# Kernel tuning notes

Measured on AMD Instinct MI355X. Metric: run time of the kernel, lower is better.

## Reference

```python
import jax, jax.numpy as jnp
import numpy as np

ATTRACTION_W = 1.0
REPULSION_W = 1.0
BETA_POS_W = 1.0
BETA_NEG_W = 0.5
K_INST = 256  # max number of distinct instance ids (slice ids)


def setup_inputs() -> dict:
    key = jax.random.key(0)
    B, N, D, K = 4, 65536, 256, K_INST
    k1, k2, k3 = jax.random.split(key, 3)
    beta = jax.random.normal(k1, (B, N, 1), jnp.float32)
    embed = jax.random.normal(k2, (B, N, D), jnp.float32)
    sid = jax.random.randint(k3, (B, N), -1, K)  # -1 = background
    # force exactly one condensation point per instance: hit i (<K) -> sid=i, is_cp
    sid = sid.at[:, :K].set(jnp.broadcast_to(jnp.arange(K), (B, K)))
    is_cp = jnp.zeros((B, N), bool).at[:, :K].set(True)
    return {"beta": beta, "embed": embed, "slice_id": sid, "is_cp": is_cp}


def _loss_single(beta, emb, sid, cp):
    # beta: (N,) logits, emb: (N,D), sid: (N,) int, cp: (N,) bool
    N = sid.shape[0]
    valid = sid >= 0
    cpv = cp & valid  # condensation points with a valid instance id
    # BCE-with-logits: target 1 -> softplus(-x), target 0 -> softplus(x)
    pos = jnp.sum(jnp.where(cpv, jax.nn.softplus(-beta), 0.0)) / jnp.maximum(cpv.sum(), 1)
    noncp = ~cp
    neg = jnp.sum(jnp.where(noncp, jax.nn.softplus(beta), 0.0)) / jnp.maximum(noncp.sum(), 1)
    beta_loss = BETA_POS_W * pos + BETA_NEG_W * neg

    # first CP hit index per instance (segment-min over CP hits), N = "no CP"
    sid_c = jnp.where(valid, sid, 0)
    idx = jnp.arange(N)
    first_cp = jnp.full((K_INST,), N, jnp.int32).at[sid_c].min(
        jnp.where(cpv, idx, N).astype(jnp.int32))
    has_cp = first_cp < N
    cp_emb = emb[jnp.minimum(first_cp, N - 1)]  # (K, D), garbage where no CP

    # attraction: sum over instances of mean ||emb - inst_cp||^2
    d2 = jnp.sum((emb - cp_emb[sid_c]) ** 2, axis=-1)  # (N,)
    w = valid & has_cp[sid_c]
    seg_sum = jnp.zeros((K_INST,), jnp.float32).at[sid_c].add(jnp.where(w, d2, 0.0))
    seg_cnt = jnp.zeros((K_INST,), jnp.float32).at[sid_c].add(w.astype(jnp.float32))
    attraction = jnp.sum(jnp.where(seg_cnt > 0, seg_sum / jnp.maximum(seg_cnt, 1.0), 0.0))
    attraction = attraction * ATTRACTION_W

    # repulsion: mean exp(-||cp_i - cp_j||^2) over all CP pairs (incl. diagonal)
    pd2 = jnp.sum((cp_emb[:, None, :] - cp_emb[None, :, :]) ** 2, axis=-1)  # (K,K)
    pmask = has_cp[:, None] & has_cp[None, :]
    M = has_cp.sum()
    rep = jnp.sum(jnp.where(pmask, jnp.exp(-pd2), 0.0)) / jnp.maximum(M * M, 1)
    rep = jnp.where(M > 1, rep * REPULSION_W, 0.0)

    loss = beta_loss + attraction + rep
    ok = (valid.sum() > 0) & (cpv.sum() > 0)
    return jnp.where(ok, loss, 0.0), ok


def reference(beta, embed, slice_id, is_cp):
    losses, oks = jax.vmap(_loss_single)(beta.squeeze(-1), embed, slice_id, is_cp)
    cnt = oks.sum()
    return jnp.where(cnt > 0, losses.sum() / jnp.maximum(cnt, 1), 0.0)
```

## Files before the change

kernel.cpp:

```cpp
#include <hip/hip_runtime.h>
#include <math.h>

#define K_INST 256
#define ATTRACTION_W 1.0f
#define REPULSION_W 1.0f
#define BETA_POS_W 1.0f
#define BETA_NEG_W 0.5f

typedef float f32x4 __attribute__((ext_vector_type(4)));

__device__ inline float softplusf(float x) {
    return fmaxf(x, 0.f) + log1pf(expf(-fabsf(x)));
}

__device__ inline float waveReduceSumF(float v) {
    for (int o = 32; o; o >>= 1) v += __shfl_xor(v, o);
    return v;
}
__device__ inline int waveReduceSumI(int v) {
    for (int o = 32; o; o >>= 1) v += __shfl_xor(v, o);
    return v;
}

__global__ void init_kernel(int* first_cp, float* seg_sum, int* seg_cnt,
                            float* pos_sum, float* neg_sum, float* rep_sum,
                            int* cpv_cnt, int* noncp_cnt, int* valid_cnt,
                            int N, int B) {
    int idx = blockIdx.x * blockDim.x + threadIdx.x;
    if (idx < B * K_INST) {
        first_cp[idx] = N;
        seg_sum[idx] = 0.f;
        seg_cnt[idx] = 0;
    }
    if (idx < B) {
        pos_sum[idx] = 0.f; neg_sum[idx] = 0.f; rep_sum[idx] = 0.f;
        cpv_cnt[idx] = 0; noncp_cnt[idx] = 0; valid_cnt[idx] = 0;
    }
}

__global__ void stats_kernel(const float* __restrict__ beta,
                             const int* __restrict__ sid,
                             const int* __restrict__ is_cp,
                             int* first_cp,
                             float* pos_sum, float* neg_sum,
                             int* cpv_cnt, int* noncp_cnt, int* valid_cnt,
                             int N) {
    int b = blockIdx.y;
    int i = blockIdx.x * blockDim.x + threadIdx.x;
    size_t gi = (size_t)b * N + i;
    int s = sid[gi];
    int cp = is_cp[gi];
    float x = beta[gi];

    bool valid = s >= 0;
    bool cpv = cp && valid;
    float pos = 0.f, neg = 0.f;
    int c_cpv = 0, c_non = 0, c_val = valid ? 1 : 0;
    if (cpv) {
        pos = softplusf(-x);
        c_cpv = 1;
        atomicMin(&first_cp[b * K_INST + s], i);
    }
    if (!cp) {
        neg = softplusf(x);
        c_non = 1;
    }

    __shared__ float sf[2][4];
    __shared__ int si[3][4];
    pos = waveReduceSumF(pos);
    neg = waveReduceSumF(neg);
    c_cpv = waveReduceSumI(c_cpv);
    c_non = waveReduceSumI(c_non);
    c_val = waveReduceSumI(c_val);
    int wave = threadIdx.x >> 6, lane = threadIdx.x & 63;
    if (lane == 0) {
        sf[0][wave] = pos; sf[1][wave] = neg;
        si[0][wave] = c_cpv; si[1][wave] = c_non; si[2][wave] = c_val;
    }
    __syncthreads();
    if (threadIdx.x == 0) {
        float p = sf[0][0] + sf[0][1] + sf[0][2] + sf[0][3];
        float n = sf[1][0] + sf[1][1] + sf[1][2] + sf[1][3];
        int a = si[0][0] + si[0][1] + si[0][2] + si[0][3];
        int c = si[1][0] + si[1][1] + si[1][2] + si[1][3];
        int v = si[2][0] + si[2][1] + si[2][2] + si[2][3];
        if (p != 0.f) atomicAdd(&pos_sum[b], p);
        if (n != 0.f) atomicAdd(&neg_sum[b], n);
        if (a) atomicAdd(&cpv_cnt[b], a);
        if (c) atomicAdd(&noncp_cnt[b], c);
        if (v) atomicAdd(&valid_cnt[b], v);
    }
}

__global__ void gather_kernel(const float* __restrict__ embed,
                              const int* __restrict__ first_cp,
                              float* __restrict__ cp_emb,
                              float* __restrict__ cp_embT, int N) {
    int b = blockIdx.y;
    int k = blockIdx.x;
    int src = first_cp[b * K_INST + k];
    if (src >= N) src = N - 1;
    int lane = threadIdx.x;
    const float* embB = embed + (size_t)b * N * 256;
    f32x4 v = ((const f32x4*)(embB + (size_t)src * 256))[lane];
    ((f32x4*)(cp_emb + ((size_t)b * K_INST + k) * 256))[lane] = v;
    float* T = cp_embT + (size_t)b * K_INST * 256;
    int d = lane * 4;
    T[(size_t)(d + 0) * 256 + k] = v[0];
    T[(size_t)(d + 1) * 256 + k] = v[1];
    T[(size_t)(d + 2) * 256 + k] = v[2];
    T[(size_t)(d + 3) * 256 + k] = v[3];
}

__device__ inline float sel8f(const float* v, int lane) {
    float a0 = (lane & 1) ? v[1] : v[0];
    float a1 = (lane & 1) ? v[3] : v[2];
    float a2 = (lane & 1) ? v[5] : v[4];
    float a3 = (lane & 1) ? v[7] : v[6];
    float b0 = (lane & 2) ? a1 : a0;
    float b1 = (lane & 2) ? a3 : a2;
    return (lane & 4) ? b1 : b0;
}
__device__ inline int sel8i(const int* v, int lane) {
    int a0 = (lane & 1) ? v[1] : v[0];
    int a1 = (lane & 1) ? v[3] : v[2];
    int a2 = (lane & 1) ? v[5] : v[4];
    int a3 = (lane & 1) ? v[7] : v[6];
    int b0 = (lane & 2) ? a1 : a0;
    int b1 = (lane & 2) ? a3 : a2;
    return (lane & 4) ? b1 : b0;
}

__global__ void attraction_repulsion_kernel(
        const float* __restrict__ embed,
        const int* __restrict__ sid,
        const int* __restrict__ first_cp,
        const float* __restrict__ cp_emb,
        const float* __restrict__ cp_embT,
        float* seg_sum, int* seg_cnt, float* rep_sum,
        int N, int atr_blocks) {
    int b = blockIdx.y;
    __shared__ __align__(16) char smem[8448];
    __shared__ float sf[4];

    const float* cpB = cp_emb + (size_t)b * K_INST * 256;
    const int* fcB = first_cp + b * K_INST;

    if (blockIdx.x < 32) {
        float (*srow)[264] = (float(*)[264])smem;
        int i0 = blockIdx.x * 8;
        const float* T = cp_embT + (size_t)b * K_INST * 256;
        {
            int r = threadIdx.x >> 5, cc = (threadIdx.x & 31) * 8;
            f32x4 a = *(const f32x4*)(cpB + (size_t)(i0 + r) * 256 + cc);
            f32x4 bv = *(const f32x4*)(cpB + (size_t)(i0 + r) * 256 + cc + 4);
            srow[r][cc + 0] = a[0]; srow[r][cc + 1] = a[1];
            srow[r][cc + 2] = a[2]; srow[r][cc + 3] = a[3];
            srow[r][cc + 4] = bv[0]; srow[r][cc + 5] = bv[1];
            srow[r][cc + 6] = bv[2]; srow[r][cc + 7] = bv[3];
        }
        __syncthreads();

        int j = threadIdx.x;
        bool has_j = fcB[j] < N;
        float acc[8] = {0.f, 0.f, 0.f, 0.f, 0.f, 0.f, 0.f, 0.f};
        for (int d = 0; d < 256; d += 2) {
            float v0 = T[(size_t)d * 256 + j];
            float v1 = T[(size_t)(d + 1) * 256 + j];
            #pragma unroll
            for (int r = 0; r < 8; ++r) {
                float f0 = srow[r][d] - v0;
                float f1 = srow[r][d + 1] - v1;
                acc[r] += f0 * f0 + f1 * f1;
            }
        }
        float val = 0.f;
        #pragma unroll
        for (int r = 0; r < 8; ++r) {
            bool has_i = fcB[i0 + r] < N;
            if (has_i && has_j) val += expf(-acc[r]);
        }
        val = waveReduceSumF(val);
        int wave = threadIdx.x >> 6, lane = threadIdx.x & 63;
        if (lane == 0) sf[wave] = val;
        __syncthreads();
        if (threadIdx.x == 0)
            atomicAdd(&rep_sum[b], sf[0] + sf[1] + sf[2] + sf[3]);
    } else {
        float* s_sum = (float*)smem;
        int* s_cnt = (int*)(smem + 1024);
        for (int k = threadIdx.x; k < K_INST; k += blockDim.x) { s_sum[k] = 0.f; s_cnt[k] = 0; }
        __syncthreads();

        int bx = blockIdx.x - 32;
        int wave = threadIdx.x >> 6;
        int lane = threadIdx.x & 63;
        int wid = bx * 4 + wave;
        int stride = atr_blocks * 4 * 8;

        const float* embB = embed + (size_t)b * N * 256;
        const int* sidB = sid + (size_t)b * N;

        int i = wid * 8;
        int4 sa = make_int4(0, 0, 0, 0), sb = make_int4(0, 0, 0, 0);
        if (i < N) {
            sa = *(const int4*)(sidB + i);
            sb = *(const int4*)(sidB + i + 4);
        }
        while (i < N) {
            int ss[8] = {sa.x, sa.y, sa.z, sa.w, sb.x, sb.y, sb.z, sb.w};

            f32x4 e[8];
            #pragma unroll
            for (int j = 0; j < 8; ++j)
                e[j] = *(const f32x4*)(embB + (size_t)(i + j) * 256 + lane * 4);
            f32x4 c[8];
            #pragma unroll
            for (int j = 0; j < 8; ++j) {
                int sc = ss[j] < 0 ? 0 : ss[j];
                c[j] = *(const f32x4*)(cpB + (size_t)sc * 256 + lane * 4);
            }
            int inext = i + stride;
            int4 na = make_int4(0, 0, 0, 0), nb = make_int4(0, 0, 0, 0);
            if (inext < N) {
                na = *(const int4*)(sidB + inext);
                nb = *(const int4*)(sidB + inext + 4);
            }

            float v[8];
            #pragma unroll
            for (int j = 0; j < 8; ++j) {
                float d0 = e[j][0] - c[j][0], d1 = e[j][1] - c[j][1];
                float d2 = e[j][2] - c[j][2], d3 = e[j][3] - c[j][3];
                v[j] = d0 * d0 + d1 * d1 + d2 * d2 + d3 * d3;
            }
            #pragma unroll
            for (int o = 1; o <= 4; o <<= 1) {
                #pragma unroll
                for (int j = 0; j < 8; ++j) v[j] += __shfl_xor(v[j], o);
            }
            float w = sel8f(v, lane & 7);
            #pragma unroll
            for (int o = 8; o <= 32; o <<= 1) w += __shfl_xor(w, o);
            if (lane < 8) {
                int s_sel = sel8i(ss, lane);
                if (s_sel >= 0) {
                    atomicAdd(&s_sum[s_sel], w);
                    atomicAdd(&s_cnt[s_sel], 1);
                }
            }
            sa = na; sb = nb;
            i = inext;
        }
        __syncthreads();
        for (int k = threadIdx.x; k < K_INST; k += blockDim.x) {
            if (s_cnt[k]) {
                atomicAdd(&seg_sum[b * K_INST + k], s_sum[k]);
                atomicAdd(&seg_cnt[b * K_INST + k], s_cnt[k]);
            }
        }
    }
}

__global__ void final_kernel(const int* __restrict__ first_cp,
                             const float* __restrict__ seg_sum,
                             const int* __restrict__ seg_cnt,
                             const float* __restrict__ pos_sum,
                             const float* __restrict__ neg_sum,
                             const float* __restrict__ rep_sum,
                             const int* __restrict__ cpv_cnt,
                             const int* __restrict__ noncp_cnt,
                             const int* __restrict__ valid_cnt,
                             float* out, int N, int B) {
    __shared__ float s_att[4];
    __shared__ int s_m[4];
    float loss_sum = 0.f;
    int ok_cnt = 0;
    int wave = threadIdx.x >> 6, lane = threadIdx.x & 63;
    for (int b = 0; b < B; ++b) {
        int k = threadIdx.x;
        int fc = first_cp[b * K_INST + k];
        int has = (fc < N) ? 1 : 0;
        int cnt = seg_cnt[b * K_INST + k];
        float att = (has && cnt > 0) ? (seg_sum[b * K_INST + k] / (float)cnt) : 0.f;
        att = waveReduceSumF(att);
        has = waveReduceSumI(has);
        if (lane == 0) { s_att[wave] = att; s_m[wave] = has; }
        __syncthreads();
        if (threadIdx.x == 0) {
            float attraction = (s_att[0] + s_att[1] + s_att[2] + s_att[3]) * ATTRACTION_W;
            int M = s_m[0] + s_m[1] + s_m[2] + s_m[3];
            float pos = pos_sum[b] / fmaxf((float)cpv_cnt[b], 1.f);
            float neg = neg_sum[b] / fmaxf((float)noncp_cnt[b], 1.f);
            float beta_loss = BETA_POS_W * pos + BETA_NEG_W * neg;
            float rep = 0.f;
            if (M > 1) {
                float mm = (float)M * (float)M;
                rep = (rep_sum[b] / fmaxf(mm, 1.f)) * REPULSION_W;
            }
            float loss = beta_loss + attraction + rep;
            bool ok = (valid_cnt[b] > 0) && (cpv_cnt[b] > 0);
            if (ok) { loss_sum += loss; ok_cnt += 1; }
        }
        __syncthreads();
    }
    if (threadIdx.x == 0) {
        out[0] = (ok_cnt > 0) ? (loss_sum / (float)ok_cnt) : 0.f;
    }
}

extern "C" void kernel_launch(void* const* d_in, const int* in_sizes, int n_in,
                              void* d_out, int out_size, void* d_ws, size_t ws_size,
                              hipStream_t stream) {
    const float* beta  = (const float*)d_in[0];
    const float* embed = (const float*)d_in[1];
    const int* sid     = (const int*)d_in[2];
    const int* is_cp   = (const int*)d_in[3];
    float* out = (float*)d_out;

    const int N = 65536;
    const int B = in_sizes[0] / N;
    (void)n_in; (void)out_size; (void)ws_size;

    char* ws = (char*)d_ws;
    int*   first_cp  = (int*)(ws + 0);
    float* seg_sum   = (float*)(ws + 4096);
    int*   seg_cnt   = (int*)(ws + 8192);
    float* pos_sum   = (float*)(ws + 12288);
    float* neg_sum   = (float*)(ws + 12352);
    float* rep_sum   = (float*)(ws + 12416);
    int*   cpv_cnt   = (int*)(ws + 12480);
    int*   noncp_cnt = (int*)(ws + 12544);
    int*   valid_cnt = (int*)(ws + 12608);
    float* cp_emb    = (float*)(ws + 16384);
    float* cp_embT   = (float*)(ws + 16384 + (size_t)B * K_INST * 256 * 4);

    init_kernel<<<dim3((B * K_INST + 255) / 256), dim3(256), 0, stream>>>(
        first_cp, seg_sum, seg_cnt, pos_sum, neg_sum, rep_sum,
        cpv_cnt, noncp_cnt, valid_cnt, N, B);

    stats_kernel<<<dim3(N / 256, B), dim3(256), 0, stream>>>(
        beta, sid, is_cp, first_cp, pos_sum, neg_sum,
        cpv_cnt, noncp_cnt, valid_cnt, N);

    gather_kernel<<<dim3(K_INST, B), dim3(64), 0, stream>>>(
        embed, first_cp, cp_emb, cp_embT, N);

    const int atr_blocks = 480;
    attraction_repulsion_kernel<<<dim3(32 + atr_blocks, B), dim3(256), 0, stream>>>(
        embed, sid, first_cp, cp_emb, cp_embT,
        seg_sum, seg_cnt, rep_sum, N, atr_blocks);

    final_kernel<<<dim3(1), dim3(256), 0, stream>>>(
        first_cp, seg_sum, seg_cnt, pos_sum, neg_sum, rep_sum,
        cpv_cnt, noncp_cnt, valid_cnt, out, N, B);
}
```

Measured before the change: 107.9 us.

## Vectorize stats kernel, use memsets, nontemporal embed loads, simpler segment reduction

Replaces the init kernel with two hipMemsetAsync calls. The 0x7F fill gives first_cp a sentinel larger than N. The stats kernel now processes four hits per thread with vector loads, so it launches a quarter as many blocks. In the attraction loop, embed and slice ids use nontemporal loads to avoid polluting the cache, and the select-based partial reduction becomes eight full wave reductions with lane 0 doing the LDS atomics. The attraction block count rises from 480 to 512. The new reduction uses more shuffles and serializes the atomics on a single lane, which may offset the other gains.

```diff
diff --git a/kernel.cpp b/kernel.cpp
--- a/kernel.cpp
+++ b/kernel.cpp
@@ -8,6 +8,7 @@
 #define BETA_NEG_W 0.5f
 
 typedef float f32x4 __attribute__((ext_vector_type(4)));
+typedef int i32x4 __attribute__((ext_vector_type(4)));
 
 __device__ inline float softplusf(float x) {
     return fmaxf(x, 0.f) + log1pf(expf(-fabsf(x)));
@@ -20,22 +21,6 @@
 __device__ inline int waveReduceSumI(int v) {
     for (int o = 32; o; o >>= 1) v += __shfl_xor(v, o);
     return v;
-}
-
-__global__ void init_kernel(int* first_cp, float* seg_sum, int* seg_cnt,
-                            float* pos_sum, float* neg_sum, float* rep_sum,
-                            int* cpv_cnt, int* noncp_cnt, int* valid_cnt,
-                            int N, int B) {
-    int idx = blockIdx.x * blockDim.x + threadIdx.x;
-    if (idx < B * K_INST) {
-        first_cp[idx] = N;
-        seg_sum[idx] = 0.f;
-        seg_cnt[idx] = 0;
-    }
-    if (idx < B) {
-        pos_sum[idx] = 0.f; neg_sum[idx] = 0.f; rep_sum[idx] = 0.f;
-        cpv_cnt[idx] = 0; noncp_cnt[idx] = 0; valid_cnt[idx] = 0;
-    }
 }
 
 __global__ void stats_kernel(const float* __restrict__ beta,
@@ -46,24 +31,33 @@
                              int* cpv_cnt, int* noncp_cnt, int* valid_cnt,
                              int N) {
     int b = blockIdx.y;
-    int i = blockIdx.x * blockDim.x + threadIdx.x;
-    size_t gi = (size_t)b * N + i;
-    int s = sid[gi];
-    int cp = is_cp[gi];
-    float x = beta[gi];
-
-    bool valid = s >= 0;
-    bool cpv = cp && valid;
+    int base = (blockIdx.x * blockDim.x + threadIdx.x) * 4;
+    const float* betaB = beta + (size_t)b * N;
+    const int* sidB = sid + (size_t)b * N;
+    const int* cpB = is_cp + (size_t)b * N;
+
+    i32x4 s4 = *(const i32x4*)(sidB + base);
+    i32x4 c4 = *(const i32x4*)(cpB + base);
+    f32x4 x4 = *(const f32x4*)(betaB + base);
+
     float pos = 0.f, neg = 0.f;
-    int c_cpv = 0, c_non = 0, c_val = valid ? 1 : 0;
-    if (cpv) {
-        pos = softplusf(-x);
-        c_cpv = 1;
-        atomicMin(&first_cp[b * K_INST + s], i);
-    }
-    if (!cp) {
-        neg = softplusf(x);
-        c_non = 1;
+    int c_cpv = 0, c_non = 0, c_val = 0;
+    #pragma unroll
+    for (int e = 0; e < 4; ++e) {
+        int s = s4[e], cp = c4[e];
+        float x = x4[e];
+        bool valid = s >= 0;
+        bool cpv = cp && valid;
+        if (cpv) {
+            pos += softplusf(-x);
+            c_cpv++;
+            atomicMin(&first_cp[b * K_INST + s], base + e);
+        }
+        if (!cp) {
+            neg += softplusf(x);
+            c_non++;
+        }
+        c_val += valid ? 1 : 0;
     }
 
     __shared__ float sf[2][4];
@@ -113,25 +107,6 @@
     T[(size_t)(d + 3) * 256 + k] = v[3];
 }
 
-__device__ inline float sel8f(const float* v, int lane) {
-    float a0 = (lane & 1) ? v[1] : v[0];
-    float a1 = (lane & 1) ? v[3] : v[2];
-    float a2 = (lane & 1) ? v[5] : v[4];
-    float a3 = (lane & 1) ? v[7] : v[6];
-    float b0 = (lane & 2) ? a1 : a0;
-    float b1 = (lane & 2) ? a3 : a2;
-    return (lane & 4) ? b1 : b0;
-}
-__device__ inline int sel8i(const int* v, int lane) {
-    int a0 = (lane & 1) ? v[1] : v[0];
-    int a1 = (lane & 1) ? v[3] : v[2];
-    int a2 = (lane & 1) ? v[5] : v[4];
-    int a3 = (lane & 1) ? v[7] : v[6];
-    int b0 = (lane & 2) ? a1 : a0;
-    int b1 = (lane & 2) ? a3 : a2;
-    return (lane & 4) ? b1 : b0;
-}
-
 __global__ void attraction_repulsion_kernel(
         const float* __restrict__ embed,
         const int* __restrict__ sid,
@@ -194,27 +169,27 @@
         __syncthreads();
 
         int bx = blockIdx.x - 32;
-        int wave = threadIdx.x >> 6;
         int lane = threadIdx.x & 63;
-        int wid = bx * 4 + wave;
+        int wid = bx * 4 + (threadIdx.x >> 6);
         int stride = atr_blocks * 4 * 8;
 
         const float* embB = embed + (size_t)b * N * 256;
         const int* sidB = sid + (size_t)b * N;
 
         int i = wid * 8;
-        int4 sa = make_int4(0, 0, 0, 0), sb = make_int4(0, 0, 0, 0);
+        i32x4 sa = {0, 0, 0, 0}, sb = {0, 0, 0, 0};
         if (i < N) {
-            sa = *(const int4*)(sidB + i);
-            sb = *(const int4*)(sidB + i + 4);
+            sa = __builtin_nontemporal_load((const i32x4*)(sidB + i));
+            sb = __builtin_nontemporal_load((const i32x4*)(sidB + i + 4));
         }
         while (i < N) {
-            int ss[8] = {sa.x, sa.y, sa.z, sa.w, sb.x, sb.y, sb.z, sb.w};
+            int ss[8] = {sa[0], sa[1], sa[2], sa[3], sb[0], sb[1], sb[2], sb[3]};
 
             f32x4 e[8];
             #pragma unroll
             for (int j = 0; j < 8; ++j)
-                e[j] = *(const f32x4*)(embB + (size_t)(i + j) * 256 + lane * 4);
+                e[j] = __builtin_nontemporal_load(
+                    (const f32x4*)(embB + (size_t)(i + j) * 256 + lane * 4));
             f32x4 c[8];
             #pragma unroll
             for (int j = 0; j < 8; ++j) {
@@ -222,10 +197,10 @@
                 c[j] = *(const f32x4*)(cpB + (size_t)sc * 256 + lane * 4);
             }
             int inext = i + stride;
-            int4 na = make_int4(0, 0, 0, 0), nb = make_int4(0, 0, 0, 0);
+            i32x4 na = {0, 0, 0, 0}, nb = {0, 0, 0, 0};
             if (inext < N) {
-                na = *(const int4*)(sidB + inext);
-                nb = *(const int4*)(sidB + inext + 4);
+                na = __builtin_nontemporal_load((const i32x4*)(sidB + inext));
+                nb = __builtin_nontemporal_load((const i32x4*)(sidB + inext + 4));
             }
 
             float v[8];
@@ -236,18 +211,14 @@
                 v[j] = d0 * d0 + d1 * d1 + d2 * d2 + d3 * d3;
             }
             #pragma unroll
-            for (int o = 1; o <= 4; o <<= 1) {
+            for (int j = 0; j < 8; ++j) v[j] = waveReduceSumF(v[j]);
+            if (lane == 0) {
                 #pragma unroll
-                for (int j = 0; j < 8; ++j) v[j] += __shfl_xor(v[j], o);
-            }
-            float w = sel8f(v, lane & 7);
-            #pragma unroll
-            for (int o = 8; o <= 32; o <<= 1) w += __shfl_xor(w, o);
-            if (lane < 8) {
-                int s_sel = sel8i(ss, lane);
-                if (s_sel >= 0) {
-                    atomicAdd(&s_sum[s_sel], w);
-                    atomicAdd(&s_cnt[s_sel], 1);
+                for (int j = 0; j < 8; ++j) {
+                    if (ss[j] >= 0) {
+                        atomicAdd(&s_sum[ss[j]], v[j]);
+                        atomicAdd(&s_cnt[ss[j]], 1);
+                    }
                 }
             }
             sa = na; sb = nb;
@@ -336,18 +307,17 @@
     float* cp_emb    = (float*)(ws + 16384);
     float* cp_embT   = (float*)(ws + 16384 + (size_t)B * K_INST * 256 * 4);
 
-    init_kernel<<<dim3((B * K_INST + 255) / 256), dim3(256), 0, stream>>>(
-        first_cp, seg_sum, seg_cnt, pos_sum, neg_sum, rep_sum,
-        cpv_cnt, noncp_cnt, valid_cnt, N, B);
-
-    stats_kernel<<<dim3(N / 256, B), dim3(256), 0, stream>>>(
+    hipMemsetAsync(first_cp, 0x7F, (size_t)B * K_INST * 4, stream);
+    hipMemsetAsync(ws + 4096, 0, 12288, stream);
+
+    stats_kernel<<<dim3(N / 1024, B), dim3(256), 0, stream>>>(
         beta, sid, is_cp, first_cp, pos_sum, neg_sum,
         cpv_cnt, noncp_cnt, valid_cnt, N);
 
     gather_kernel<<<dim3(K_INST, B), dim3(64), 0, stream>>>(
         embed, first_cp, cp_emb, cp_embT, N);
 
-    const int atr_blocks = 480;
+    const int atr_blocks = 512;
     attraction_repulsion_kernel<<<dim3(32 + atr_blocks, B), dim3(256), 0, stream>>>(
         embed, sid, first_cp, cp_emb, cp_embT,
         seg_sum, seg_cnt, rep_sum, N, atr_blocks);
```

After: 98.70 us, median of 2. -8.5%, faster.
